# Kernel tuning notes

Measured on AMD Instinct MI355X. Metric: run time of the kernel, lower is better.

Reference implementation:

```python
import jax, jax.numpy as jnp
import numpy as np

B, N, D = 8, 2048, 512

def setup_inputs() -> dict:
    key = jax.random.key(0)
    ks = jax.random.split(key, 8)
    s = 1.0 / np.sqrt(D)
    return {
        "inputs": jax.random.normal(ks[0], (B, N, D), dtype=jnp.float32),
        "mask": jnp.ones((B, N), dtype=jnp.int32),
        "Wk": jax.random.normal(ks[1], (D, D), dtype=jnp.float32) * s,
        "bk": jax.random.normal(ks[2], (D,), dtype=jnp.float32) * s,
        "Wq": jax.random.normal(ks[3], (D, D), dtype=jnp.float32) * s,
        "bq": jax.random.normal(ks[4], (D,), dtype=jnp.float32) * s,
        "Wv": jax.random.normal(ks[5], (D, D), dtype=jnp.float32) * s,
        "bv": jax.random.normal(ks[6], (D,), dtype=jnp.float32) * s,
    }

def reference(inputs, mask, Wk, bk, Wq, bq, Wv, bv):
    # torch Linear: y = x @ W.T + b
    keys = jnp.einsum('bnd,ed->bne', inputs, Wk) + bk
    queries = jnp.einsum('bnd,ed->bne', inputs, Wq) + bq
    values = jnp.einsum('bnd,ed->bne', inputs, Wv) + bv
    norm = jnp.sqrt(jnp.asarray(D, inputs.dtype))
    scores = jnp.einsum('bqd,bkd->bqk', queries, keys) / norm  # [B,N,N]
    scores = jnp.where(mask[:, None, :] == 0, jnp.asarray(-1e9, scores.dtype), scores)
    attn = jax.nn.softmax(scores, axis=-1)
    return jnp.einsum('bqk,bkd->bqd', attn, values)
```

## Files before the change

### kernel.cpp

```cpp
#include <hip/hip_runtime.h>
#include <hip/hip_bf16.h>


typedef __attribute__((ext_vector_type(8))) short short8;
typedef __attribute__((ext_vector_type(4))) float f32x4;

#define DEV __device__ __forceinline__
#define GLOBAL_AS __attribute__((address_space(1)))
#define LDS_AS __attribute__((address_space(3)))

static DEV ushort f2bs(float f) {
  union { float f; unsigned u; } x; x.f = f;
  unsigned r = (x.u + 0x7fffu + ((x.u >> 16) & 1u)) >> 16;
  return (ushort)r;
}

static DEV f32x4 mfma16(short8 a, short8 b, f32x4 c) {
  return __builtin_amdgcn_mfma_f32_16x16x32_bf16(a, b, c, 0, 0, 0);
}

static DEV void async16(const void* g, void* l) {
  __builtin_amdgcn_global_load_lds((const GLOBAL_AS void*)g, (LDS_AS void*)l, 16, 0, 0);
}

__global__ void convert_all(const float* __restrict__ wq, const float* __restrict__ wk,
                            const float* __restrict__ wv, const float* __restrict__ x,
                            ushort* __restrict__ wb, ushort* __restrict__ xb,
                            float* __restrict__ lde) {
  int i = blockIdx.x * 256 + threadIdx.x;
  if (i >= 2293760) {
    int off = (i - 2293760) * 4;
    float4 z; z.x = 0.f; z.y = 0.f; z.z = 0.f; z.w = 0.f;
    *(float4*)(lde + off) = z;
    return;
  }
  const float* src;
  ushort* dst;
  if (i < 196608) {
    int which = i >> 16;
    int off = (i & 65535) * 4;
    src = ((which == 0) ? wq : (which == 1) ? wk : wv) + off;
    dst = wb + (size_t)which * 262144 + off;
  } else {
    int off = (i - 196608) * 4;
    src = x + off;
    dst = xb + off;
  }
  float4 v = *(const float4*)src;
  ushort4 o;
  o.x = f2bs(v.x); o.y = f2bs(v.y); o.z = f2bs(v.z); o.w = f2bs(v.w);
  *(ushort4*)dst = o;
}

#define KLOOP_STAGE(Aptr, lda, Bptr, ldb)                                      \
  do {                                                                         \
    _Pragma("unroll")                                                          \
    for (int t = 0; t < 8; t++) {                                              \
      int rowbase = (t & 3) * 32 + wave * 8;                                   \
      int r = rowbase + (lane >> 3);                                           \
      int gc = (lane & 7) ^ (r & 7);                                           \
      if (t < 4)                                                               \
        async16((Aptr) + (size_t)(rowblk * 128 + r) * (lda) + kb + gc * 8,     \
                &As[rowbase * 64]);                                            \
      else                                                                     \
        async16((Bptr) + (size_t)(colblk * 128 + r) * (ldb) + kb + gc * 8,     \
                &Bs[rowbase * 64]);                                            \
    }                                                                          \
  } while (0)

#define KLOOP_MFMA()                                                           \
  do {                                                                         \
    _Pragma("unroll")                                                          \
    for (int ks = 0; ks < 2; ks++) {                                           \
      short8 af[4], bfr[4];                                                    \
      _Pragma("unroll")                                                        \
      for (int t = 0; t < 4; t++) {                                            \
        int ra = wm * 64 + t * 16 + c16;                                       \
        int rb = wn * 64 + t * 16 + c16;                                       \
        af[t]  = *(const short8*)&As[ra * 64 + (((ks * 4 + quad) ^ (ra & 7)) * 8)]; \
        bfr[t] = *(const short8*)&Bs[rb * 64 + (((ks * 4 + quad) ^ (rb & 7)) * 8)]; \
      }                                                                        \
      _Pragma("unroll")                                                        \
      for (int mt = 0; mt < 4; mt++)                                           \
        _Pragma("unroll")                                                      \
        for (int nt = 0; nt < 4; nt++)                                         \
          acc[mt][nt] = mfma16(af[mt], bfr[nt], acc[mt][nt]);                  \
    }                                                                          \
  } while (0)

__launch_bounds__(256, 4)
__global__ void qkv_gemm(const ushort* __restrict__ Xb, const ushort* __restrict__ Wb,
                         const float* __restrict__ bq, const float* __restrict__ bk,
                         const float* __restrict__ bv,
                         ushort* __restrict__ Qb, ushort* __restrict__ Kb,
                         ushort* __restrict__ Vtb) {
  const int rowblk = blockIdx.x;
  const int colblk = blockIdx.y;
  const int z = colblk >> 2;

  __shared__ ushort S[2 * 128 * 64];
  ushort* As = S;
  ushort* Bs = S + 128 * 64;

  const int tid = threadIdx.x;
  const int wave = tid >> 6, lane = tid & 63, quad = lane >> 4, c16 = lane & 15;
  const int wm = wave & 1, wn = wave >> 1;

  f32x4 acc[4][4];
#pragma unroll
  for (int mt = 0; mt < 4; mt++)
#pragma unroll
    for (int nt = 0; nt < 4; nt++) acc[mt][nt] = (f32x4)0.0f;

  for (int kb = 0; kb < 512; kb += 64) {
    __syncthreads();
    KLOOP_STAGE(Xb, 512, Wb, 512);
    __syncthreads();
    KLOOP_MFMA();
  }

  const float* bias = (z == 0) ? bq : (z == 1) ? bk : bv;
  float bvals[4];
#pragma unroll
  for (int nt = 0; nt < 4; nt++) {
    int eg = colblk * 128 + wn * 64 + nt * 16 + c16;
    bvals[nt] = bias[eg & 511];
  }
  const float sc = (z == 0) ? 0.044194173824159216f : 1.0f;

  const int row0 = rowblk * 128 + wm * 64;
  const int col0 = colblk * 128 + wn * 64;
  if (z < 2) {
    ushort* O = (z == 0) ? Qb : Kb;
#pragma unroll
    for (int mt = 0; mt < 4; mt++)
#pragma unroll
      for (int nt = 0; nt < 4; nt++) {
        int el = (col0 + nt * 16 + c16) & 511;
#pragma unroll
        for (int r = 0; r < 4; r++) {
          int n = row0 + mt * 16 + quad * 4 + r;
          O[(size_t)n * 512 + el] = f2bs((acc[mt][nt][r] + bvals[nt]) * sc);
        }
      }
  } else {
    __syncthreads();
    ushort* T = S;
#pragma unroll
    for (int nt = 0; nt < 4; nt++) {
      int ell = wn * 64 + nt * 16 + c16;
#pragma unroll
      for (int mt = 0; mt < 4; mt++) {
        int n0l = wm * 64 + mt * 16 + quad * 4;
        ushort4 o;
        o.x = f2bs(acc[mt][nt][0] + bvals[nt]);
        o.y = f2bs(acc[mt][nt][1] + bvals[nt]);
        o.z = f2bs(acc[mt][nt][2] + bvals[nt]);
        o.w = f2bs(acc[mt][nt][3] + bvals[nt]);
        *(ushort4*)&T[ell * 128 + (((n0l >> 3) ^ (ell & 15)) << 3) + (n0l & 4)] = o;
      }
    }
    __syncthreads();
    const int c4 = tid & 3, er = tid >> 2;
    const int bb = rowblk >> 4;
    const int nbase = (rowblk & 15) * 128;
    const int elbase = (colblk & 3) * 128;
#pragma unroll
    for (int part = 0; part < 2; part++) {
      int ell = part * 64 + er;
      size_t ge = ((size_t)bb * 512 + elbase + ell) * 2048;
#pragma unroll
      for (int j2 = 0; j2 < 4; j2++) {
        int n0 = j2 * 32 + c4 * 8;
        short8 v = *(short8*)&T[ell * 128 + (((n0 >> 3) ^ (ell & 15)) << 3)];
        *(short8*)(Vtb + ge + nbase + n0) = v;
      }
    }
  }
}

__launch_bounds__(256, 4)
__global__ void gemm_s(const ushort* __restrict__ Kb, const ushort* __restrict__ Qb,
                       const int* __restrict__ mask, ushort* __restrict__ Pm,
                       float* __restrict__ l) {
  const int b = blockIdx.z;
  const int rowblk = blockIdx.x;
  const int colblk = blockIdx.y;
  const ushort* A  = Kb + (size_t)b * 2048 * 512;
  const ushort* Bq = Qb + (size_t)b * 2048 * 512;

  __shared__ ushort S[2 * 128 * 64];
  ushort* As = S;
  ushort* Bs = S + 128 * 64;

  const int tid = threadIdx.x;
  const int wave = tid >> 6, lane = tid & 63, quad = lane >> 4, c16 = lane & 15;
  const int wm = wave & 1, wn = wave >> 1;

  f32x4 acc[4][4];
#pragma unroll
  for (int mt = 0; mt < 4; mt++)
#pragma unroll
    for (int nt = 0; nt < 4; nt++) acc[mt][nt] = (f32x4)0.0f;

  for (int kb = 0; kb < 512; kb += 64) {
    __syncthreads();
    KLOOP_STAGE(A, 512, Bq, 512);
    __syncthreads();
    KLOOP_MFMA();
  }

  const int row0 = rowblk * 128 + wm * 64;
  const int col0 = colblk * 128 + wn * 64;
  float lpart[4] = {0.0f, 0.0f, 0.0f, 0.0f};

  __syncthreads();
  ushort* T = S;
#pragma unroll
  for (int mt = 0; mt < 4; mt++) {
    int key0 = row0 + mt * 16 + quad * 4;
    int k0l  = wm * 64 + mt * 16 + quad * 4;
    int4 mv = *(const int4*)&mask[b * 2048 + key0];
    float mf0 = mv.x ? 1.0f : 0.0f, mf1 = mv.y ? 1.0f : 0.0f;
    float mf2 = mv.z ? 1.0f : 0.0f, mf3 = mv.w ? 1.0f : 0.0f;
#pragma unroll
    for (int nt = 0; nt < 4; nt++) {
      int ql = wn * 64 + nt * 16 + c16;
      float p0 = __expf(acc[mt][nt][0]) * mf0;
      float p1 = __expf(acc[mt][nt][1]) * mf1;
      float p2 = __expf(acc[mt][nt][2]) * mf2;
      float p3 = __expf(acc[mt][nt][3]) * mf3;
      ushort4 o;
      o.x = f2bs(p0); o.y = f2bs(p1); o.z = f2bs(p2); o.w = f2bs(p3);
      *(ushort4*)&T[ql * 128 + (((k0l >> 3) ^ (ql & 15)) << 3) + (k0l & 4)] = o;
      lpart[nt] += p0 + p1 + p2 + p3;
    }
  }
#pragma unroll
  for (int nt = 0; nt < 4; nt++) {
    float v = lpart[nt];
    v += __shfl_xor(v, 16, 64);
    v += __shfl_xor(v, 32, 64);
    if (quad == 0) atomicAdd(&l[b * 2048 + col0 + nt * 16 + c16], v);
  }
  __syncthreads();
  {
    const int c4 = tid & 3, er = tid >> 2;
#pragma unroll
    for (int part = 0; part < 2; part++) {
      int ql = part * 64 + er;
      size_t gq = ((size_t)b * 2048 + colblk * 128 + ql) * 2048;
#pragma unroll
      for (int j2 = 0; j2 < 4; j2++) {
        int n0 = j2 * 32 + c4 * 8;
        short8 v = *(short8*)&T[ql * 128 + (((n0 >> 3) ^ (ql & 15)) << 3)];
        *(short8*)(Pm + gq + rowblk * 128 + n0) = v;
      }
    }
  }
}

#define OST_A(pp, kt, rd)                                                      \
  do {                                                                         \
    int rowbase_ = (rd) * 64 + wave * 8;                                       \
    int r_ = rowbase_ + (lane >> 3);                                           \
    int gc_ = (lane & 7) ^ (r_ & 7);                                           \
    async16(A + (size_t)(rowblk * 256 + r_) * 2048 + (kt) * 64 + gc_ * 8,      \
            SdA + (pp) * 16384 + rowbase_ * 64);                               \
  } while (0)

#define OST_B(pp, kt, rd)                                                      \
  do {                                                                         \
    int rowbase_ = (rd) * 64 + wave * 8;                                       \
    int r_ = rowbase_ + (lane >> 3);                                           \
    int gc_ = (lane & 7) ^ (r_ & 7);                                           \
    async16(Bv + (size_t)(colblk * 128 + r_) * 2048 + (kt) * 64 + gc_ * 8,     \
            SdB + (pp) * 8192 + rowbase_ * 64);                                \
  } while (0)

#define OREAD(pp, ks, afx, bfx)                                                \
  do {                                                                         \
    const ushort* Ap_ = SdA + (pp) * 16384;                                    \
    const ushort* Bp_ = SdB + (pp) * 8192;                                     \
    _Pragma("unroll")                                                          \
    for (int mf = 0; mf < 4; mf++) {                                           \
      int ra = wm * 64 + mf * 16 + c16;                                        \
      afx[mf] = *(const short8*)&Ap_[ra * 64 + ((((ks)*4 + quad) ^ (ra & 7)) * 8)]; \
    }                                                                          \
    _Pragma("unroll")                                                          \
    for (int nf = 0; nf < 4; nf++) {                                           \
      int rb = wn * 64 + nf * 16 + c16;                                        \
      bfx[nf] = *(const short8*)&Bp_[rb * 64 + ((((ks)*4 + quad) ^ (rb & 7)) * 8)]; \
    }                                                                          \
  } while (0)

#define OMFMA(afx, bfx, h)                                                     \
  do {                                                                         \
    __builtin_amdgcn_s_setprio(1);                                             \
    _Pragma("unroll")                                                          \
    for (int mf = (h) * 2; mf < (h) * 2 + 2; mf++)                             \
      _Pragma("unroll")                                                        \
      for (int nf = 0; nf < 4; nf++)                                           \
        acc[mf][nf] = mfma16(afx[mf], bfx[nf], acc[mf][nf]);                   \
    __builtin_amdgcn_s_setprio(0);                                             \
  } while (0)

#define OTILE(pp, kt, dostage)                                                 \
  do {                                                                         \
    OREAD(pp, 0, af0, bf0);                                                    \
    __builtin_amdgcn_s_barrier();                                              \
    asm volatile("s_waitcnt lgkmcnt(0)" ::: "memory");                         \
    __builtin_amdgcn_sched_barrier(0);                                         \
    OMFMA(af0, bf0, 0);                                                        \
    __builtin_amdgcn_s_barrier();                                              \
    OREAD(pp, 1, af1, bf1);                                                    \
    __builtin_amdgcn_s_barrier();                                              \
    asm volatile("s_waitcnt lgkmcnt(0)" ::: "memory");                         \
    __builtin_amdgcn_sched_barrier(0);                                         \
    OMFMA(af0, bf0, 1);                                                        \
    __builtin_amdgcn_s_barrier();         \
    if (dostage) { OST_A(pp, (kt) + 2, 0); OST_A(pp, (kt) + 2, 1);             \
                   OST_A(pp, (kt) + 2, 2); }                                   \
    OMFMA(af1, bf1, 0);                                                        \
    __builtin_amdgcn_s_barrier();                                              \
    if (dostage) { OST_A(pp, (kt) + 2, 3); OST_B(pp, (kt) + 2, 0);             \
                   OST_B(pp, (kt) + 2, 1); }                                   \
    OMFMA(af1, bf1, 1);                                                        \
    if (dostage) { asm volatile("s_waitcnt vmcnt(6)" ::: "memory"); }          \
    else         { asm volatile("s_waitcnt vmcnt(0)" ::: "memory"); }          \
    __builtin_amdgcn_sched_barrier(0);                                         \
    __builtin_amdgcn_s_barrier();        \
  } while (0)

__launch_bounds__(512, 2)
__global__ void gemm_o(const ushort* __restrict__ Pm, const ushort* __restrict__ Vtb,
                       const float* __restrict__ l, float* __restrict__ out) {
  const int bid = blockIdx.x;
  const int b = bid & 7;
  const int rowblk = (bid >> 3) & 7;
  const int colblk = bid >> 6;
  const ushort* A  = Pm  + (size_t)b * 2048 * 2048;
  const ushort* Bv = Vtb + (size_t)b * 512 * 2048;

  extern __shared__ ushort Sd[];
  ushort* SdA = Sd;
  ushort* SdB = Sd + 32768;

  const int tid = threadIdx.x;
  const int wave = tid >> 6, lane = tid & 63, quad = lane >> 4, c16 = lane & 15;
  const int wm = wave >> 1, wn = wave & 1;

  f32x4 acc[4][4];
#pragma unroll
  for (int mf = 0; mf < 4; mf++)
#pragma unroll
    for (int nf = 0; nf < 4; nf++) acc[mf][nf] = (f32x4)0.0f;

  OST_A(0, 0, 0); OST_A(0, 0, 1); OST_A(0, 0, 2); OST_A(0, 0, 3);
  OST_B(0, 0, 0); OST_B(0, 0, 1);
  OST_A(1, 1, 0); OST_A(1, 1, 1); OST_A(1, 1, 2); OST_A(1, 1, 3);
  OST_B(1, 1, 0); OST_B(1, 1, 1);
  asm volatile("s_waitcnt vmcnt(6)" ::: "memory");
  __builtin_amdgcn_sched_barrier(0);
  __builtin_amdgcn_s_barrier();

  short8 af0[4], bf0[4], af1[4], bf1[4];
  for (int i = 0; i < 16; i++) {
    const int dostage = (i < 15);
    OTILE(0, 2 * i, dostage);
    OTILE(1, 2 * i + 1, dostage);
  }

  const int row0 = rowblk * 256 + wm * 64;
  const int col0 = colblk * 128 + wn * 64;
  float linv[4][4];
#pragma unroll
  for (int mf = 0; mf < 4; mf++)
#pragma unroll
    for (int r = 0; r < 4; r++)
      linv[mf][r] = 1.0f / l[b * 2048 + row0 + mf * 16 + quad * 4 + r];
#pragma unroll
  for (int mf = 0; mf < 4; mf++)
#pragma unroll
    for (int nf = 0; nf < 4; nf++) {
      int col = col0 + nf * 16 + c16;
#pragma unroll
      for (int r = 0; r < 4; r++) {
        int row = row0 + mf * 16 + quad * 4 + r;
        out[((size_t)b * 2048 + row) * 512 + col] = acc[mf][nf][r] * linv[mf][r];
      }
    }
}

extern "C" void kernel_launch(void* const* d_in, const int* in_sizes, int n_in,
                              void* d_out, int out_size, void* d_ws, size_t ws_size,
                              hipStream_t stream) {
  (void)in_sizes; (void)n_in; (void)out_size; (void)ws_size;
  const float* X    = (const float*)d_in[0];
  const int*   mask = (const int*)d_in[1];
  const float* Wk   = (const float*)d_in[2];
  const float* bk   = (const float*)d_in[3];
  const float* Wq   = (const float*)d_in[4];
  const float* bq   = (const float*)d_in[5];
  const float* Wv   = (const float*)d_in[6];
  const float* bv   = (const float*)d_in[7];
  float* out = (float*)d_out;

  ushort* ws  = (ushort*)d_ws;
  ushort* Pm  = ws;
  ushort* Xb  = ws;
  ushort* Wb  = ws + (size_t)33554432;
  ushort* Qb  = Wb + (size_t)786432;
  ushort* Kb  = Qb + (size_t)8388608;
  ushort* Vtb = Kb + (size_t)8388608;
  float*  lde = (float*)(Vtb + (size_t)8388608);

  convert_all<<<8976, 256, 0, stream>>>(Wq, Wk, Wv, X, Wb, Xb, lde);
  qkv_gemm<<<dim3(128, 12), 256, 0, stream>>>(Xb, Wb, bq, bk, bv, Qb, Kb, Vtb);
  gemm_s<<<dim3(16, 16, 8), 256, 0, stream>>>(Kb, Qb, mask, Pm, lde);
  gemm_o<<<256, 512, 98304, stream>>>(Pm, Vtb, lde, out);
}
```

Baseline: 204.7 us.

## Reuse pipelined 256x128 double-buffered GEMM core for QKV and score kernels

Generalizes gemm_o's software-pipelined, double-buffered async LDS staging and MFMA schedule into shared macros and applies it to the QKV projection and the score/exp kernels. Both now use 512-thread blocks with 256x128 tiles and 96KB dynamic LDS, replacing the simple sync-load-compute loop. The goal is to overlap global loads with MFMA and raise data reuse per tile. The cost is fewer, larger blocks, which may reduce occupancy and load balance, especially for the short K=512 loops.

Measured after the change: 218.8 us. 6.9% more time.

```diff
diff --git a/kernel.cpp b/kernel.cpp
--- a/kernel.cpp
+++ b/kernel.cpp
@@ -52,233 +52,25 @@
   *(ushort4*)dst = o;
 }
 
-#define KLOOP_STAGE(Aptr, lda, Bptr, ldb)                                      \
-  do {                                                                         \
-    _Pragma("unroll")                                                          \
-    for (int t = 0; t < 8; t++) {                                              \
-      int rowbase = (t & 3) * 32 + wave * 8;                                   \
-      int r = rowbase + (lane >> 3);                                           \
-      int gc = (lane & 7) ^ (r & 7);                                           \
-      if (t < 4)                                                               \
-        async16((Aptr) + (size_t)(rowblk * 128 + r) * (lda) + kb + gc * 8,     \
-                &As[rowbase * 64]);                                            \
-      else                                                                     \
-        async16((Bptr) + (size_t)(colblk * 128 + r) * (ldb) + kb + gc * 8,     \
-                &Bs[rowbase * 64]);                                            \
-    }                                                                          \
-  } while (0)
-
-#define KLOOP_MFMA()                                                           \
-  do {                                                                         \
-    _Pragma("unroll")                                                          \
-    for (int ks = 0; ks < 2; ks++) {                                           \
-      short8 af[4], bfr[4];                                                    \
-      _Pragma("unroll")                                                        \
-      for (int t = 0; t < 4; t++) {                                            \
-        int ra = wm * 64 + t * 16 + c16;                                       \
-        int rb = wn * 64 + t * 16 + c16;                                       \
-        af[t]  = *(const short8*)&As[ra * 64 + (((ks * 4 + quad) ^ (ra & 7)) * 8)]; \
-        bfr[t] = *(const short8*)&Bs[rb * 64 + (((ks * 4 + quad) ^ (rb & 7)) * 8)]; \
-      }                                                                        \
-      _Pragma("unroll")                                                        \
-      for (int mt = 0; mt < 4; mt++)                                           \
-        _Pragma("unroll")                                                      \
-        for (int nt = 0; nt < 4; nt++)                                         \
-          acc[mt][nt] = mfma16(af[mt], bfr[nt], acc[mt][nt]);                  \
-    }                                                                          \
-  } while (0)
-
-__launch_bounds__(256, 4)
-__global__ void qkv_gemm(const ushort* __restrict__ Xb, const ushort* __restrict__ Wb,
-                         const float* __restrict__ bq, const float* __restrict__ bk,
-                         const float* __restrict__ bv,
-                         ushort* __restrict__ Qb, ushort* __restrict__ Kb,
-                         ushort* __restrict__ Vtb) {
-  const int rowblk = blockIdx.x;
-  const int colblk = blockIdx.y;
-  const int z = colblk >> 2;
-
-  __shared__ ushort S[2 * 128 * 64];
-  ushort* As = S;
-  ushort* Bs = S + 128 * 64;
-
-  const int tid = threadIdx.x;
-  const int wave = tid >> 6, lane = tid & 63, quad = lane >> 4, c16 = lane & 15;
-  const int wm = wave & 1, wn = wave >> 1;
-
-  f32x4 acc[4][4];
-#pragma unroll
-  for (int mt = 0; mt < 4; mt++)
-#pragma unroll
-    for (int nt = 0; nt < 4; nt++) acc[mt][nt] = (f32x4)0.0f;
-
-  for (int kb = 0; kb < 512; kb += 64) {
-    __syncthreads();
-    KLOOP_STAGE(Xb, 512, Wb, 512);
-    __syncthreads();
-    KLOOP_MFMA();
-  }
-
-  const float* bias = (z == 0) ? bq : (z == 1) ? bk : bv;
-  float bvals[4];
-#pragma unroll
-  for (int nt = 0; nt < 4; nt++) {
-    int eg = colblk * 128 + wn * 64 + nt * 16 + c16;
-    bvals[nt] = bias[eg & 511];
-  }
-  const float sc = (z == 0) ? 0.044194173824159216f : 1.0f;
-
-  const int row0 = rowblk * 128 + wm * 64;
-  const int col0 = colblk * 128 + wn * 64;
-  if (z < 2) {
-    ushort* O = (z == 0) ? Qb : Kb;
-#pragma unroll
-    for (int mt = 0; mt < 4; mt++)
-#pragma unroll
-      for (int nt = 0; nt < 4; nt++) {
-        int el = (col0 + nt * 16 + c16) & 511;
-#pragma unroll
-        for (int r = 0; r < 4; r++) {
-          int n = row0 + mt * 16 + quad * 4 + r;
-          O[(size_t)n * 512 + el] = f2bs((acc[mt][nt][r] + bvals[nt]) * sc);
-        }
-      }
-  } else {
-    __syncthreads();
-    ushort* T = S;
-#pragma unroll
-    for (int nt = 0; nt < 4; nt++) {
-      int ell = wn * 64 + nt * 16 + c16;
-#pragma unroll
-      for (int mt = 0; mt < 4; mt++) {
-        int n0l = wm * 64 + mt * 16 + quad * 4;
-        ushort4 o;
-        o.x = f2bs(acc[mt][nt][0] + bvals[nt]);
-        o.y = f2bs(acc[mt][nt][1] + bvals[nt]);
-        o.z = f2bs(acc[mt][nt][2] + bvals[nt]);
-        o.w = f2bs(acc[mt][nt][3] + bvals[nt]);
-        *(ushort4*)&T[ell * 128 + (((n0l >> 3) ^ (ell & 15)) << 3) + (n0l & 4)] = o;
-      }
-    }
-    __syncthreads();
-    const int c4 = tid & 3, er = tid >> 2;
-    const int bb = rowblk >> 4;
-    const int nbase = (rowblk & 15) * 128;
-    const int elbase = (colblk & 3) * 128;
-#pragma unroll
-    for (int part = 0; part < 2; part++) {
-      int ell = part * 64 + er;
-      size_t ge = ((size_t)bb * 512 + elbase + ell) * 2048;
-#pragma unroll
-      for (int j2 = 0; j2 < 4; j2++) {
-        int n0 = j2 * 32 + c4 * 8;
-        short8 v = *(short8*)&T[ell * 128 + (((n0 >> 3) ^ (ell & 15)) << 3)];
-        *(short8*)(Vtb + ge + nbase + n0) = v;
-      }
-    }
-  }
-}
-
-__launch_bounds__(256, 4)
-__global__ void gemm_s(const ushort* __restrict__ Kb, const ushort* __restrict__ Qb,
-                       const int* __restrict__ mask, ushort* __restrict__ Pm,
-                       float* __restrict__ l) {
-  const int b = blockIdx.z;
-  const int rowblk = blockIdx.x;
-  const int colblk = blockIdx.y;
-  const ushort* A  = Kb + (size_t)b * 2048 * 512;
-  const ushort* Bq = Qb + (size_t)b * 2048 * 512;
-
-  __shared__ ushort S[2 * 128 * 64];
-  ushort* As = S;
-  ushort* Bs = S + 128 * 64;
-
-  const int tid = threadIdx.x;
-  const int wave = tid >> 6, lane = tid & 63, quad = lane >> 4, c16 = lane & 15;
-  const int wm = wave & 1, wn = wave >> 1;
-
-  f32x4 acc[4][4];
-#pragma unroll
-  for (int mt = 0; mt < 4; mt++)
-#pragma unroll
-    for (int nt = 0; nt < 4; nt++) acc[mt][nt] = (f32x4)0.0f;
-
-  for (int kb = 0; kb < 512; kb += 64) {
-    __syncthreads();
-    KLOOP_STAGE(A, 512, Bq, 512);
-    __syncthreads();
-    KLOOP_MFMA();
-  }
-
-  const int row0 = rowblk * 128 + wm * 64;
-  const int col0 = colblk * 128 + wn * 64;
-  float lpart[4] = {0.0f, 0.0f, 0.0f, 0.0f};
-
-  __syncthreads();
-  ushort* T = S;
-#pragma unroll
-  for (int mt = 0; mt < 4; mt++) {
-    int key0 = row0 + mt * 16 + quad * 4;
-    int k0l  = wm * 64 + mt * 16 + quad * 4;
-    int4 mv = *(const int4*)&mask[b * 2048 + key0];
-    float mf0 = mv.x ? 1.0f : 0.0f, mf1 = mv.y ? 1.0f : 0.0f;
-    float mf2 = mv.z ? 1.0f : 0.0f, mf3 = mv.w ? 1.0f : 0.0f;
-#pragma unroll
-    for (int nt = 0; nt < 4; nt++) {
-      int ql = wn * 64 + nt * 16 + c16;
-      float p0 = __expf(acc[mt][nt][0]) * mf0;
-      float p1 = __expf(acc[mt][nt][1]) * mf1;
-      float p2 = __expf(acc[mt][nt][2]) * mf2;
-      float p3 = __expf(acc[mt][nt][3]) * mf3;
-      ushort4 o;
-      o.x = f2bs(p0); o.y = f2bs(p1); o.z = f2bs(p2); o.w = f2bs(p3);
-      *(ushort4*)&T[ql * 128 + (((k0l >> 3) ^ (ql & 15)) << 3) + (k0l & 4)] = o;
-      lpart[nt] += p0 + p1 + p2 + p3;
-    }
-  }
-#pragma unroll
-  for (int nt = 0; nt < 4; nt++) {
-    float v = lpart[nt];
-    v += __shfl_xor(v, 16, 64);
-    v += __shfl_xor(v, 32, 64);
-    if (quad == 0) atomicAdd(&l[b * 2048 + col0 + nt * 16 + c16], v);
-  }
-  __syncthreads();
-  {
-    const int c4 = tid & 3, er = tid >> 2;
-#pragma unroll
-    for (int part = 0; part < 2; part++) {
-      int ql = part * 64 + er;
-      size_t gq = ((size_t)b * 2048 + colblk * 128 + ql) * 2048;
-#pragma unroll
-      for (int j2 = 0; j2 < 4; j2++) {
-        int n0 = j2 * 32 + c4 * 8;
-        short8 v = *(short8*)&T[ql * 128 + (((n0 >> 3) ^ (ql & 15)) << 3)];
-        *(short8*)(Pm + gq + rowblk * 128 + n0) = v;
-      }
-    }
-  }
-}
-
-#define OST_A(pp, kt, rd)                                                      \
+#define PH_ST_A(pp, kt, rd)                                                    \
   do {                                                                         \
     int rowbase_ = (rd) * 64 + wave * 8;                                       \
     int r_ = rowbase_ + (lane >> 3);                                           \
     int gc_ = (lane & 7) ^ (r_ & 7);                                           \
-    async16(A + (size_t)(rowblk * 256 + r_) * 2048 + (kt) * 64 + gc_ * 8,      \
+    async16(gA + (size_t)(arow0 + r_) * glda + (kt) * 64 + gc_ * 8,            \
             SdA + (pp) * 16384 + rowbase_ * 64);                               \
   } while (0)
 
-#define OST_B(pp, kt, rd)                                                      \
+#define PH_ST_B(pp, kt, rd)                                                    \
   do {                                                                         \
     int rowbase_ = (rd) * 64 + wave * 8;                                       \
     int r_ = rowbase_ + (lane >> 3);                                           \
     int gc_ = (lane & 7) ^ (r_ & 7);                                           \
-    async16(Bv + (size_t)(colblk * 128 + r_) * 2048 + (kt) * 64 + gc_ * 8,     \
+    async16(gB + (size_t)(brow0 + r_) * gldb + (kt) * 64 + gc_ * 8,            \
             SdB + (pp) * 8192 + rowbase_ * 64);                                \
   } while (0)
 
-#define OREAD(pp, ks, afx, bfx)                                                \
+#define PH_READ(pp, ks, afx, bfx)                                              \
   do {                                                                         \
     const ushort* Ap_ = SdA + (pp) * 16384;                                    \
     const ushort* Bp_ = SdB + (pp) * 8192;                                     \
@@ -294,7 +86,7 @@
     }                                                                          \
   } while (0)
 
-#define OMFMA(afx, bfx, h)                                                     \
+#define PH_MFMA(afx, bfx, h)                                                   \
   do {                                                                         \
     __builtin_amdgcn_s_setprio(1);                                             \
     _Pragma("unroll")                                                          \
@@ -305,32 +97,210 @@
     __builtin_amdgcn_s_setprio(0);                                             \
   } while (0)
 
-#define OTILE(pp, kt, dostage)                                                 \
-  do {                                                                         \
-    OREAD(pp, 0, af0, bf0);                                                    \
+#define PH_TILE(pp, kt, dostage)                                               \
+  do {                                                                         \
+    PH_READ(pp, 0, af0, bf0);                                                  \
     __builtin_amdgcn_s_barrier();                                              \
     asm volatile("s_waitcnt lgkmcnt(0)" ::: "memory");                         \
     __builtin_amdgcn_sched_barrier(0);                                         \
-    OMFMA(af0, bf0, 0);                                                        \
-    __builtin_amdgcn_s_barrier();                                              \
-    OREAD(pp, 1, af1, bf1);                                                    \
+    PH_MFMA(af0, bf0, 0);                                                      \
+    __builtin_amdgcn_s_barrier();                                              \
+    PH_READ(pp, 1, af1, bf1);                                                  \
     __builtin_amdgcn_s_barrier();                                              \
     asm volatile("s_waitcnt lgkmcnt(0)" ::: "memory");                         \
     __builtin_amdgcn_sched_barrier(0);                                         \
-    OMFMA(af0, bf0, 1);                                                        \
+    PH_MFMA(af0, bf0, 1);                                                      \
     __builtin_amdgcn_s_barrier();         \
-    if (dostage) { OST_A(pp, (kt) + 2, 0); OST_A(pp, (kt) + 2, 1);             \
-                   OST_A(pp, (kt) + 2, 2); }                                   \
-    OMFMA(af1, bf1, 0);                                                        \
-    __builtin_amdgcn_s_barrier();                                              \
-    if (dostage) { OST_A(pp, (kt) + 2, 3); OST_B(pp, (kt) + 2, 0);             \
-                   OST_B(pp, (kt) + 2, 1); }                                   \
-    OMFMA(af1, bf1, 1);                                                        \
+    if (dostage) { PH_ST_A(pp, (kt) + 2, 0); PH_ST_A(pp, (kt) + 2, 1);         \
+                   PH_ST_A(pp, (kt) + 2, 2); }                                 \
+    PH_MFMA(af1, bf1, 0);                                                      \
+    __builtin_amdgcn_s_barrier();                                              \
+    if (dostage) { PH_ST_A(pp, (kt) + 2, 3); PH_ST_B(pp, (kt) + 2, 0);         \
+                   PH_ST_B(pp, (kt) + 2, 1); }                                 \
+    PH_MFMA(af1, bf1, 1);                                                      \
     if (dostage) { asm volatile("s_waitcnt vmcnt(6)" ::: "memory"); }          \
     else         { asm volatile("s_waitcnt vmcnt(0)" ::: "memory"); }          \
     __builtin_amdgcn_sched_barrier(0);                                         \
     __builtin_amdgcn_s_barrier();        \
   } while (0)
+
+#define PH_PROLOGUE()                                                          \
+  do {                                                                         \
+    PH_ST_A(0, 0, 0); PH_ST_A(0, 0, 1); PH_ST_A(0, 0, 2); PH_ST_A(0, 0, 3);    \
+    PH_ST_B(0, 0, 0); PH_ST_B(0, 0, 1);                                        \
+    PH_ST_A(1, 1, 0); PH_ST_A(1, 1, 1); PH_ST_A(1, 1, 2); PH_ST_A(1, 1, 3);    \
+    PH_ST_B(1, 1, 0); PH_ST_B(1, 1, 1);                                        \
+    asm volatile("s_waitcnt vmcnt(6)" ::: "memory");                           \
+    __builtin_amdgcn_sched_barrier(0);                                         \
+    __builtin_amdgcn_s_barrier();                                              \
+  } while (0)
+
+__launch_bounds__(512, 2)
+__global__ void qkv_gemm(const ushort* __restrict__ Xb, const ushort* __restrict__ Wb,
+                         const float* __restrict__ bq, const float* __restrict__ bk,
+                         const float* __restrict__ bv,
+                         ushort* __restrict__ Qb, ushort* __restrict__ Kb,
+                         ushort* __restrict__ Vtb) {
+  const int rowblk = blockIdx.x;
+  const int colblk = blockIdx.y;
+  const int z = colblk >> 2;
+
+  extern __shared__ ushort Sd[];
+  ushort* SdA = Sd;
+  ushort* SdB = Sd + 32768;
+
+  const int tid = threadIdx.x;
+  const int wave = tid >> 6, lane = tid & 63, quad = lane >> 4, c16 = lane & 15;
+  const int wm = wave >> 1, wn = wave & 1;
+
+  const ushort* gA = Xb;  const int glda = 512; const int arow0 = rowblk * 256;
+  const ushort* gB = Wb;  const int gldb = 512; const int brow0 = colblk * 128;
+
+  f32x4 acc[4][4];
+#pragma unroll
+  for (int mf = 0; mf < 4; mf++)
+#pragma unroll
+    for (int nf = 0; nf < 4; nf++) acc[mf][nf] = (f32x4)0.0f;
+
+  PH_PROLOGUE();
+  short8 af0[4], bf0[4], af1[4], bf1[4];
+  for (int i = 0; i < 4; i++) {
+    const int ds = (i < 3);
+    PH_TILE(0, 2 * i, ds);
+    PH_TILE(1, 2 * i + 1, ds);
+  }
+
+  const float* bias = (z == 0) ? bq : (z == 1) ? bk : bv;
+  const int col0 = (colblk & 3) * 128 + wn * 64;
+  float bvals[4];
+#pragma unroll
+  for (int nf = 0; nf < 4; nf++) bvals[nf] = bias[col0 + nf * 16 + c16];
+  const float sc = (z == 0) ? 0.044194173824159216f : 1.0f;
+
+  const int row0 = rowblk * 256 + wm * 64;
+  if (z < 2) {
+    ushort* O = (z == 0) ? Qb : Kb;
+#pragma unroll
+    for (int mf = 0; mf < 4; mf++)
+#pragma unroll
+      for (int nf = 0; nf < 4; nf++) {
+        int el = col0 + nf * 16 + c16;
+#pragma unroll
+        for (int r = 0; r < 4; r++) {
+          int n = row0 + mf * 16 + quad * 4 + r;
+          O[(size_t)n * 512 + el] = f2bs((acc[mf][nf][r] + bvals[nf]) * sc);
+        }
+      }
+  } else {
+    __syncthreads();
+    ushort* T = Sd;
+#pragma unroll
+    for (int nf = 0; nf < 4; nf++) {
+      int ell = wn * 64 + nf * 16 + c16;
+#pragma unroll
+      for (int mf = 0; mf < 4; mf++) {
+        int n0 = wm * 64 + mf * 16 + quad * 4;
+        ushort4 o;
+        o.x = f2bs(acc[mf][nf][0] + bvals[nf]);
+        o.y = f2bs(acc[mf][nf][1] + bvals[nf]);
+        o.z = f2bs(acc[mf][nf][2] + bvals[nf]);
+        o.w = f2bs(acc[mf][nf][3] + bvals[nf]);
+        *(ushort4*)&T[ell * 256 + (((n0 >> 3) ^ (ell & 31)) << 3) + (n0 & 4)] = o;
+      }
+    }
+    __syncthreads();
+    const int b = rowblk >> 3;
+    const int nbase = (rowblk & 7) * 256;
+    const int elbase = (colblk & 3) * 128;
+    const int c4 = tid & 3, er = tid >> 2;
+    size_t ge = ((size_t)b * 512 + elbase + er) * 2048;
+#pragma unroll
+    for (int j = 0; j < 8; j++) {
+      int ch = j * 4 + c4;
+      short8 v = *(short8*)&T[er * 256 + ((ch ^ (er & 31)) << 3)];
+      *(short8*)(Vtb + ge + nbase + ch * 8) = v;
+    }
+  }
+}
+
+__launch_bounds__(512, 2)
+__global__ void gemm_s(const ushort* __restrict__ Kb, const ushort* __restrict__ Qb,
+                       const int* __restrict__ mask, ushort* __restrict__ Pm,
+                       float* __restrict__ l) {
+  const int bid = blockIdx.x;
+  const int b = bid & 7;
+  const int rowblk = (bid >> 3) & 7;
+  const int colblk = bid >> 6;
+
+  extern __shared__ ushort Sd[];
+  ushort* SdA = Sd;
+  ushort* SdB = Sd + 32768;
+
+  const int tid = threadIdx.x;
+  const int wave = tid >> 6, lane = tid & 63, quad = lane >> 4, c16 = lane & 15;
+  const int wm = wave >> 1, wn = wave & 1;
+
+  const ushort* gA = Kb + (size_t)b * 2048 * 512;  const int glda = 512;
+  const int arow0 = rowblk * 256;
+  const ushort* gB = Qb + (size_t)b * 2048 * 512;  const int gldb = 512;
+  const int brow0 = colblk * 128;
+
+  f32x4 acc[4][4];
+#pragma unroll
+  for (int mf = 0; mf < 4; mf++)
+#pragma unroll
+    for (int nf = 0; nf < 4; nf++) acc[mf][nf] = (f32x4)0.0f;
+
+  PH_PROLOGUE();
+  short8 af0[4], bf0[4], af1[4], bf1[4];
+  for (int i = 0; i < 4; i++) {
+    const int ds = (i < 3);
+    PH_TILE(0, 2 * i, ds);
+    PH_TILE(1, 2 * i + 1, ds);
+  }
+
+  float lpart[4] = {0.0f, 0.0f, 0.0f, 0.0f};
+  __syncthreads();
+  ushort* T = Sd;
+#pragma unroll
+  for (int mf = 0; mf < 4; mf++) {
+    int keyl = wm * 64 + mf * 16 + quad * 4;
+    int4 mv = *(const int4*)&mask[b * 2048 + rowblk * 256 + keyl];
+    float m0 = mv.x ? 1.0f : 0.0f, m1 = mv.y ? 1.0f : 0.0f;
+    float m2 = mv.z ? 1.0f : 0.0f, m3 = mv.w ? 1.0f : 0.0f;
+#pragma unroll
+    for (int nf = 0; nf < 4; nf++) {
+      int ql = wn * 64 + nf * 16 + c16;
+      float p0 = __expf(acc[mf][nf][0]) * m0;
+      float p1 = __expf(acc[mf][nf][1]) * m1;
+      float p2 = __expf(acc[mf][nf][2]) * m2;
+      float p3 = __expf(acc[mf][nf][3]) * m3;
+      ushort4 o;
+      o.x = f2bs(p0); o.y = f2bs(p1); o.z = f2bs(p2); o.w = f2bs(p3);
+      *(ushort4*)&T[ql * 256 + (((keyl >> 3) ^ (ql & 31)) << 3) + (keyl & 4)] = o;
+      lpart[nf] += p0 + p1 + p2 + p3;
+    }
+  }
+#pragma unroll
+  for (int nf = 0; nf < 4; nf++) {
+    float v = lpart[nf];
+    v += __shfl_xor(v, 16, 64);
+    v += __shfl_xor(v, 32, 64);
+    if (quad == 0)
+      atomicAdd(&l[b * 2048 + colblk * 128 + wn * 64 + nf * 16 + c16], v);
+  }
+  __syncthreads();
+  {
+    const int c4 = tid & 3, er = tid >> 2;
+    size_t gq = ((size_t)b * 2048 + colblk * 128 + er) * 2048;
+#pragma unroll
+    for (int j = 0; j < 8; j++) {
+      int ch = j * 4 + c4;
+      short8 v = *(short8*)&T[er * 256 + ((ch ^ (er & 31)) << 3)];
+      *(short8*)(Pm + gq + rowblk * 256 + ch * 8) = v;
+    }
+  }
+}
 
 __launch_bounds__(512, 2)
 __global__ void gemm_o(const ushort* __restrict__ Pm, const ushort* __restrict__ Vtb,
@@ -339,8 +309,6 @@
   const int b = bid & 7;
   const int rowblk = (bid >> 3) & 7;
   const int colblk = bid >> 6;
-  const ushort* A  = Pm  + (size_t)b * 2048 * 2048;
-  const ushort* Bv = Vtb + (size_t)b * 512 * 2048;
 
   extern __shared__ ushort Sd[];
   ushort* SdA = Sd;
@@ -350,25 +318,23 @@
   const int wave = tid >> 6, lane = tid & 63, quad = lane >> 4, c16 = lane & 15;
   const int wm = wave >> 1, wn = wave & 1;
 
+  const ushort* gA = Pm + (size_t)b * 2048 * 2048;  const int glda = 2048;
+  const int arow0 = rowblk * 256;
+  const ushort* gB = Vtb + (size_t)b * 512 * 2048;  const int gldb = 2048;
+  const int brow0 = colblk * 128;
+
   f32x4 acc[4][4];
 #pragma unroll
   for (int mf = 0; mf < 4; mf++)
 #pragma unroll
     for (int nf = 0; nf < 4; nf++) acc[mf][nf] = (f32x4)0.0f;
 
-  OST_A(0, 0, 0); OST_A(0, 0, 1); OST_A(0, 0, 2); OST_A(0, 0, 3);
-  OST_B(0, 0, 0); OST_B(0, 0, 1);
-  OST_A(1, 1, 0); OST_A(1, 1, 1); OST_A(1, 1, 2); OST_A(1, 1, 3);
-  OST_B(1, 1, 0); OST_B(1, 1, 1);
-  asm volatile("s_waitcnt vmcnt(6)" ::: "memory");
-  __builtin_amdgcn_sched_barrier(0);
-  __builtin_amdgcn_s_barrier();
-
+  PH_PROLOGUE();
   short8 af0[4], bf0[4], af1[4], bf1[4];
   for (int i = 0; i < 16; i++) {
-    const int dostage = (i < 15);
-    OTILE(0, 2 * i, dostage);
-    OTILE(1, 2 * i + 1, dostage);
+    const int ds = (i < 15);
+    PH_TILE(0, 2 * i, ds);
+    PH_TILE(1, 2 * i + 1, ds);
   }
 
   const int row0 = rowblk * 256 + wm * 64;
@@ -416,7 +382,7 @@
   float*  lde = (float*)(Vtb + (size_t)8388608);
 
   convert_all<<<8976, 256, 0, stream>>>(Wq, Wk, Wv, X, Wb, Xb, lde);
-  qkv_gemm<<<dim3(128, 12), 256, 0, stream>>>(Xb, Wb, bq, bk, bv, Qb, Kb, Vtb);
-  gemm_s<<<dim3(16, 16, 8), 256, 0, stream>>>(Kb, Qb, mask, Pm, lde);
+  qkv_gemm<<<dim3(64, 12), 512, 98304, stream>>>(Xb, Wb, bq, bk, bv, Qb, Kb, Vtb);
+  gemm_s<<<1024, 512, 98304, stream>>>(Kb, Qb, mask, Pm, lde);
   gemm_o<<<256, 512, 98304, stream>>>(Pm, Vtb, lde, out);
 }
```
